# Performance work log

Hardware: AMD Instinct MI355X
Metric: run time of the kernel (lower is better)

## Reference

```python
import jax, jax.numpy as jnp
import numpy as np

IN_F = 128
OUT_F = 64
ALPHA = 0.2  # LeakyReLU negative slope


def setup_inputs() -> dict:
    key = jax.random.key(0)
    k1, k2, k3 = jax.random.split(key, 3)
    B, N = 8, 2048
    inp = jax.random.normal(k1, (B, N, IN_F), dtype=jnp.float32)
    adj = jnp.ones((B, N, N), dtype=jnp.float32)  # unused by the layer (no masking)
    # Parameters (xavier_uniform-style scale)
    w_lim = np.sqrt(6.0 / (IN_F + OUT_F))
    W = jax.random.uniform(k2, (OUT_F, IN_F), minval=-w_lim, maxval=w_lim, dtype=jnp.float32)
    a_lim = np.sqrt(6.0 / (2 * OUT_F + 1))
    a = jax.random.uniform(k3, (1, 2 * OUT_F), minval=-a_lim, maxval=a_lim, dtype=jnp.float32)
    return {"input": inp, "adj": adj, "W": W, "a": a}


def reference(input, adj, W, a):
    # h = W(input): [B, N, OUT_F]
    h = jnp.einsum("bnf,of->bno", input, W)
    # a^T [h_i || h_j] = a1^T h_i + a2^T h_j  (exact decomposition of the concat trick)
    a1 = a[0, :OUT_F]
    a2 = a[0, OUT_F:]
    s1 = jnp.einsum("bno,o->bn", h, a1)  # score contribution from node i
    s2 = jnp.einsum("bno,o->bn", h, a2)  # score contribution from node j
    e = s1[:, :, None] + s2[:, None, :]  # [B, N, N]
    e = jnp.where(e >= 0, e, ALPHA * e)  # LeakyReLU
    attention = jax.nn.softmax(e, axis=2)  # softmax over neighbors j (adj is NOT used)
    h_prime = jnp.einsum("bij,bjo->bio", attention, h)
    # concat=True -> ELU
    return jax.nn.elu(h_prime)
```

## Files before the change

kernel.cpp:

```cpp
#include <hip/hip_runtime.h>
#include <cstdio>

#define ALPHA 0.2f
constexpr int NN = 2048;
constexpr int FI = 128;
constexpr int FO = 64;
constexpr int SEG = 64;
constexpr int NSEG = NN / SEG;

__global__ __launch_bounds__(256) void k_h(const float* __restrict__ inp,
    const float* __restrict__ W, const float* __restrict__ a,
    float* __restrict__ h, float* __restrict__ s1, float* __restrict__ s2)
{
  __shared__ float4 Wq[(FI / 4) * FO];
  const int t = threadIdx.x;
  const float4* Wg = (const float4*)W;
#pragma unroll
  for (int i = 0; i < 8; ++i) {
    int f = t + i * 256;
    int o = f >> 5, cq = f & 31;
    Wq[cq * FO + o] = Wg[f];
  }
  __syncthreads();
  const int lane = t & 63;
  const int wv = t >> 6;
  const size_t rowbase = ((size_t)blockIdx.x * 4 + wv) * 8;
  const float a1v = a[lane], a2v = a[FO + lane];
#pragma unroll
  for (int g = 0; g < 2; ++g) {
    const size_t r0 = rowbase + g * 4;
    const float4* x0 = (const float4*)(inp + r0 * FI);
    const float4* x1 = x0 + (FI / 4);
    const float4* x2 = x0 + 2 * (FI / 4);
    const float4* x3 = x0 + 3 * (FI / 4);
    float acc0 = 0.f, acc1 = 0.f, acc2 = 0.f, acc3 = 0.f;
#pragma unroll
    for (int cq = 0; cq < 32; ++cq) {
      float4 w = Wq[cq * FO + lane];
      float4 xa = x0[cq];
      acc0 = fmaf(xa.x, w.x, fmaf(xa.y, w.y, fmaf(xa.z, w.z, fmaf(xa.w, w.w, acc0))));
      float4 xb = x1[cq];
      acc1 = fmaf(xb.x, w.x, fmaf(xb.y, w.y, fmaf(xb.z, w.z, fmaf(xb.w, w.w, acc1))));
      float4 xc = x2[cq];
      acc2 = fmaf(xc.x, w.x, fmaf(xc.y, w.y, fmaf(xc.z, w.z, fmaf(xc.w, w.w, acc2))));
      float4 xd = x3[cq];
      acc3 = fmaf(xd.x, w.x, fmaf(xd.y, w.y, fmaf(xd.z, w.z, fmaf(xd.w, w.w, acc3))));
    }
    h[(r0 + 0) * FO + lane] = acc0;
    h[(r0 + 1) * FO + lane] = acc1;
    h[(r0 + 2) * FO + lane] = acc2;
    h[(r0 + 3) * FO + lane] = acc3;
    float p0 = acc0 * a1v, q0 = acc0 * a2v;
    float p1 = acc1 * a1v, q1 = acc1 * a2v;
    float p2 = acc2 * a1v, q2 = acc2 * a2v;
    float p3 = acc3 * a1v, q3 = acc3 * a2v;
#pragma unroll
    for (int off = 32; off; off >>= 1) {
      p0 += __shfl_down(p0, off); q0 += __shfl_down(q0, off);
      p1 += __shfl_down(p1, off); q1 += __shfl_down(q1, off);
      p2 += __shfl_down(p2, off); q2 += __shfl_down(q2, off);
      p3 += __shfl_down(p3, off); q3 += __shfl_down(q3, off);
    }
    if (lane == 0) {
      s1[r0 + 0] = p0; s2[r0 + 0] = q0;
      s1[r0 + 1] = p1; s2[r0 + 1] = q1;
      s1[r0 + 2] = p2; s2[r0 + 2] = q2;
      s1[r0 + 3] = p3; s2[r0 + 3] = q3;
    }
  }
}

__global__ __launch_bounds__(256) void k_rankA(const float* __restrict__ s2,
    int* __restrict__ part)
{
  __shared__ float ck[64];
  const int b = blockIdx.x >> 5;
  const int c = blockIdx.x & 31;
  const int t = threadIdx.x;
  if (t < 64) ck[t] = s2[b * NN + c * 64 + t];
  float v[8];
#pragma unroll
  for (int rr = 0; rr < 8; ++rr) v[rr] = s2[b * NN + rr * 256 + t];
  __syncthreads();
  int cnt[8] = {0, 0, 0, 0, 0, 0, 0, 0};
  const int j0 = c * 64;
#pragma unroll 4
  for (int jj = 0; jj < 64; ++jj) {
    const float x = ck[jj];
    const int j = j0 + jj;
#pragma unroll
    for (int rr = 0; rr < 8; ++rr) {
      const int i = rr * 256 + t;
      cnt[rr] += (x > v[rr]) || (x == v[rr] && j < i);
    }
  }
  int* pp = part + (size_t)(b * 32 + c) * NN;
#pragma unroll
  for (int rr = 0; rr < 8; ++rr) pp[rr * 256 + t] = cnt[rr];
}

__global__ __launch_bounds__(1024) void k_batch(const float* __restrict__ s2,
    const int* __restrict__ part, const float* __restrict__ s1g,
    float* __restrict__ sortedS2, int* __restrict__ sortedIdx,
    float* __restrict__ ep, float* __restrict__ eq,
    float* __restrict__ Zp, float* __restrict__ Zq,
    int* __restrict__ kArr, float* __restrict__ m2g)
{
  __shared__ float ssv[NN];
  __shared__ int sid[NN];
  __shared__ float sep[NN], seq[NN];
  __shared__ float wt[16], wo[16];
  const int b = blockIdx.x;
  const int t = threadIdx.x;
  const int lane = t & 63;
  const int w = t >> 6;
#pragma unroll
  for (int rr = 0; rr < 2; ++rr) {
    const int i = t + rr * 1024;
    const int* pp = part + (size_t)b * 32 * NN + i;
    int rank = 0;
#pragma unroll 8
    for (int c = 0; c < 32; ++c) rank += pp[(size_t)c * NN];
    float v = s2[b * NN + i];
    ssv[rank] = v;
    sid[rank] = i;
  }
  __syncthreads();
  const float m2 = ssv[0];
  if (t == 0) m2g[b] = m2;
#pragma unroll
  for (int rr = 0; rr < 2; ++rr) {
    const int r = t + rr * 1024;
    float v = ssv[r];
    float e1 = expf(v - m2), e2 = expf(ALPHA * (v - m2));
    sep[r] = e1; seq[r] = e2;
    sortedS2[b * NN + r] = v;
    sortedIdx[b * NN + r] = sid[r];
    ep[b * NN + r] = e1;
    eq[b * NN + r] = e2;
  }
  __syncthreads();
  float a0 = sep[2 * t], a1 = sep[2 * t + 1];
  float l = a0 + a1;
  float incl = l;
#pragma unroll
  for (int off = 1; off < 64; off <<= 1) {
    float x = __shfl_up(incl, off);
    if (lane >= off) incl += x;
  }
  if (lane == 63) wt[w] = incl;
  __syncthreads();
  if (t < 16) {
    float v = wt[t];
    float wi = v;
#pragma unroll
    for (int off = 1; off < 16; off <<= 1) {
      float x = __shfl_up(wi, off);
      if (t >= off) wi += x;
    }
    wo[t] = wi - v;
  }
  __syncthreads();
  {
    float excl = wo[w] + (incl - l);
    Zp[b * (NN + 1) + 2 * t] = excl;
    Zp[b * (NN + 1) + 2 * t + 1] = excl + a0;
    if (t == 1023) Zp[b * (NN + 1) + NN] = excl + l;
  }
  __syncthreads();
  float b0 = seq[NN - 1 - 2 * t], b1 = seq[NN - 2 - 2 * t];
  float l2 = b0 + b1;
  float incl2 = l2;
#pragma unroll
  for (int off = 1; off < 64; off <<= 1) {
    float x = __shfl_up(incl2, off);
    if (lane >= off) incl2 += x;
  }
  if (lane == 63) wt[w] = incl2;
  __syncthreads();
  if (t < 16) {
    float v = wt[t];
    float wi = v;
#pragma unroll
    for (int off = 1; off < 16; off <<= 1) {
      float x = __shfl_up(wi, off);
      if (t >= off) wi += x;
    }
    wo[t] = wi - v;
  }
  __syncthreads();
  {
    float excl = wo[w] + (incl2 - l2);
    Zq[b * (NN + 1) + NN - 1 - 2 * t] = excl + b0;
    Zq[b * (NN + 1) + NN - 2 - 2 * t] = excl + l2;
    if (t == 0) Zq[b * (NN + 1) + NN] = 0.f;
  }
#pragma unroll
  for (int rr = 0; rr < 2; ++rr) {
    const int i = 2 * t + rr;
    const float thr = -s1g[b * NN + i];
    int lo = 0, hi = NN;
    while (lo < hi) {
      int mid = (lo + hi) >> 1;
      if (ssv[mid] >= thr) lo = mid + 1; else hi = mid;
    }
    kArr[b * NN + i] = lo;
  }
}

__global__ __launch_bounds__(256) void k_seg(const float* __restrict__ h,
    const int* __restrict__ sortedIdx, const float* __restrict__ ep,
    const float* __restrict__ eq,
    float* __restrict__ Lp, float* __restrict__ Lq,
    float* __restrict__ segTotP, float* __restrict__ segTotQ)
{
  const int lane = threadIdx.x & 63;
  const int s = blockIdx.x * 4 + (threadIdx.x >> 6);
  const int b = s >> 5;
  const int base = b * NN + (s & (NSEG - 1)) * SEG;
  float vq[SEG];
  float runP = 0.f;
#pragma unroll
  for (int r = 0; r < SEG; ++r) {
    int idx = sortedIdx[base + r];
    float hv = h[((size_t)(b * NN + idx)) * FO + lane];
    runP = fmaf(ep[base + r], hv, runP);
    Lp[(size_t)(base + r) * FO + lane] = runP;
    vq[r] = eq[base + r] * hv;
  }
  segTotP[(size_t)s * FO + lane] = runP;
  float runQ = 0.f;
#pragma unroll
  for (int r = SEG - 1; r >= 0; --r) {
    runQ += vq[r];
    Lq[(size_t)(base + r) * FO + lane] = runQ;
  }
  segTotQ[(size_t)s * FO + lane] = runQ;
}

__global__ __launch_bounds__(256) void k_out(const float* __restrict__ s1g,
    const int* __restrict__ kArr,
    const float* __restrict__ Lp, const float* __restrict__ Lq,
    const float* __restrict__ Zp, const float* __restrict__ Zq,
    const float* __restrict__ segTotP, const float* __restrict__ segTotQ,
    const float* __restrict__ m2g, float* __restrict__ out)
{
  __shared__ float cp[NSEG][FO];
  __shared__ float cq[NSEG][FO];
  const int t = threadIdx.x;
  const int b = blockIdx.x >> 7;
  const float* stP = segTotP + (size_t)b * NSEG * FO;
  const float* stQ = segTotQ + (size_t)b * NSEG * FO;
#pragma unroll
  for (int i = 0; i < NSEG * FO / 256; ++i) {
    ((float*)cp)[t + i * 256] = stP[t + i * 256];
    ((float*)cq)[t + i * 256] = stQ[t + i * 256];
  }
  __syncthreads();
  if (t < 64) {
    float run = 0.f;
    for (int ss = 0; ss < NSEG; ++ss) { run += cp[ss][t]; cp[ss][t] = run; }
  } else if (t < 128) {
    int o = t - 64;
    float run = 0.f;
    for (int ss = NSEG - 1; ss >= 0; --ss) { run += cq[ss][o]; cq[ss][o] = run; }
  }
  __syncthreads();
  const int lane = t & 63;
  const int wv = t >> 6;
  const float m2 = m2g[b];
#pragma unroll
  for (int rr = 0; rr < 4; ++rr) {
    const int i = (blockIdx.x & 127) * 16 + wv * 4 + rr;
    const int gi = b * NN + i;
    const int k = kArr[gi];
    const float s1v = s1g[gi];
    const float u = s1v + m2;
    const float c = fmaxf(u, ALPHA * u);
    const float wp = expf(u - c);
    const float wq = expf(ALPHA * u - c);
    const float zp = Zp[b * (NN + 1) + k];
    const float zq = Zq[b * (NN + 1) + k];
    float P = 0.f, Q = 0.f;
    if (k > 0) {
      int sP = (k - 1) >> 6;
      P = (sP > 0 ? cp[sP - 1][lane] : 0.f) +
          Lp[((size_t)b * NN + (k - 1)) * FO + lane];
    }
    if (k < NN) {
      int sQ = k >> 6;
      Q = (sQ < NSEG - 1 ? cq[sQ + 1][lane] : 0.f) +
          Lq[((size_t)b * NN + k) * FO + lane];
    }
    const float v = (wp * P + wq * Q) / (wp * zp + wq * zq);
    out[(size_t)gi * FO + lane] = (v > 0.f) ? v : expm1f(v);
  }
}

extern "C" void kernel_launch(void* const* d_in, const int* in_sizes, int n_in,
                              void* d_out, int out_size, void* d_ws, size_t ws_size,
                              hipStream_t stream) {
  const float* inp = (const float*)d_in[0];
  const float* W = (const float*)d_in[2];
  const float* a = (const float*)d_in[3];
  float* out = (float*)d_out;

  constexpr size_t NH = (size_t)8 * NN * FO;
  constexpr size_t NR = (size_t)8 * NN;
  constexpr size_t NZ = (size_t)8 * (NN + 1);
  constexpr size_t NST = (size_t)8 * NSEG * FO;
  constexpr size_t needFloats = 3 * NH + 7 * NR + 2 * NZ + 2 * NST + 8 + 32 * NR;
  if (ws_size < needFloats * sizeof(float)) {
    fprintf(stderr, "kernel_launch: ws too small (%zu < %zu)\n",
            ws_size, needFloats * sizeof(float));
    return;
  }
  float* ws = (float*)d_ws;
  float* h        = ws;
  float* Lp       = h + NH;
  float* Lq       = Lp + NH;
  float* s1       = Lq + NH;
  float* s2       = s1 + NR;
  float* sortedS2 = s2 + NR;
  int*   sortedIdx= (int*)(sortedS2 + NR);
  float* ep       = (float*)(sortedIdx + NR);
  float* eq       = ep + NR;
  int*   kArr     = (int*)(eq + NR);
  float* Zp       = (float*)(kArr + NR);
  float* Zq       = Zp + NZ;
  float* segTotP  = Zq + NZ;
  float* segTotQ  = segTotP + NST;
  float* m2       = segTotQ + NST;
  int*   part     = (int*)(m2 + 8);

  k_h<<<512, 256, 0, stream>>>(inp, W, a, h, s1, s2);
  k_rankA<<<256, 256, 0, stream>>>(s2, part);
  k_batch<<<8, 1024, 0, stream>>>(s2, part, s1, sortedS2, sortedIdx, ep, eq,
                                  Zp, Zq, kArr, m2);
  k_seg<<<64, 256, 0, stream>>>(h, sortedIdx, ep, eq, Lp, Lq, segTotP, segTotQ);
  k_out<<<1024, 256, 0, stream>>>(s1, kArr, Lp, Lq, Zp, Zq,
                                  segTotP, segTotQ, m2, out);
}
```

Before: 66.80 us.

## Shrink scan segments to raise parallelism in segmented prefix-sum kernels

Reduces the segment length of the sorted prefix-sum pass from 64 to 16, so k_seg launches four times as many waves, each with a much shorter serial chain, and front-loads all gathered loads before the scans. k_out now scans the larger segment-total table with all four waves using a two-level scan instead of two serial threads, and processes twice as many rows per block with half the blocks. The unused sortedS2 write is dropped from k_batch. The trade-off is a larger segment-total table to load and scan in every k_out block, plus more register arrays per thread in k_seg.

```diff
diff --git a/kernel.cpp b/kernel.cpp
--- a/kernel.cpp
+++ b/kernel.cpp
@@ -5,7 +5,7 @@
 constexpr int NN = 2048;
 constexpr int FI = 128;
 constexpr int FO = 64;
-constexpr int SEG = 64;
+constexpr int SEG = 16;
 constexpr int NSEG = NN / SEG;
 
 __global__ __launch_bounds__(256) void k_h(const float* __restrict__ inp,
@@ -101,7 +101,7 @@
 
 __global__ __launch_bounds__(1024) void k_batch(const float* __restrict__ s2,
     const int* __restrict__ part, const float* __restrict__ s1g,
-    float* __restrict__ sortedS2, int* __restrict__ sortedIdx,
+    int* __restrict__ sortedIdx,
     float* __restrict__ ep, float* __restrict__ eq,
     float* __restrict__ Zp, float* __restrict__ Zq,
     int* __restrict__ kArr, float* __restrict__ m2g)
@@ -134,7 +134,6 @@
     float v = ssv[r];
     float e1 = expf(v - m2), e2 = expf(ALPHA * (v - m2));
     sep[r] = e1; seq[r] = e2;
-    sortedS2[b * NN + r] = v;
     sortedIdx[b * NN + r] = sid[r];
     ep[b * NN + r] = e1;
     eq[b * NN + r] = e2;
@@ -216,26 +215,30 @@
 {
   const int lane = threadIdx.x & 63;
   const int s = blockIdx.x * 4 + (threadIdx.x >> 6);
-  const int b = s >> 5;
+  const int b = s >> 7;
   const int base = b * NN + (s & (NSEG - 1)) * SEG;
-  float vq[SEG];
-  float runP = 0.f;
+  float hv[SEG], wp[SEG], wq[SEG];
 #pragma unroll
   for (int r = 0; r < SEG; ++r) {
     int idx = sortedIdx[base + r];
-    float hv = h[((size_t)(b * NN + idx)) * FO + lane];
-    runP = fmaf(ep[base + r], hv, runP);
-    Lp[(size_t)(base + r) * FO + lane] = runP;
-    vq[r] = eq[base + r] * hv;
-  }
-  segTotP[(size_t)s * FO + lane] = runP;
-  float runQ = 0.f;
+    hv[r] = h[((size_t)(b * NN + idx)) * FO + lane];
+  }
+#pragma unroll
+  for (int r = 0; r < SEG; ++r) { wp[r] = ep[base + r]; wq[r] = eq[base + r]; }
+  float run = 0.f;
+#pragma unroll
+  for (int r = 0; r < SEG; ++r) {
+    run = fmaf(wp[r], hv[r], run);
+    Lp[(size_t)(base + r) * FO + lane] = run;
+  }
+  segTotP[(size_t)s * FO + lane] = run;
+  run = 0.f;
 #pragma unroll
   for (int r = SEG - 1; r >= 0; --r) {
-    runQ += vq[r];
-    Lq[(size_t)(base + r) * FO + lane] = runQ;
-  }
-  segTotQ[(size_t)s * FO + lane] = runQ;
+    run = fmaf(wq[r], hv[r], run);
+    Lq[(size_t)(base + r) * FO + lane] = run;
+  }
+  segTotQ[(size_t)s * FO + lane] = run;
 }
 
 __global__ __launch_bounds__(256) void k_out(const float* __restrict__ s1g,
@@ -247,31 +250,44 @@
 {
   __shared__ float cp[NSEG][FO];
   __shared__ float cq[NSEG][FO];
+  __shared__ float qtP[4][FO], qtQ[4][FO];
   const int t = threadIdx.x;
-  const int b = blockIdx.x >> 7;
-  const float* stP = segTotP + (size_t)b * NSEG * FO;
-  const float* stQ = segTotQ + (size_t)b * NSEG * FO;
-#pragma unroll
-  for (int i = 0; i < NSEG * FO / 256; ++i) {
-    ((float*)cp)[t + i * 256] = stP[t + i * 256];
-    ((float*)cq)[t + i * 256] = stQ[t + i * 256];
-  }
-  __syncthreads();
-  if (t < 64) {
+  const int b = blockIdx.x >> 6;
+  const float4* stP = (const float4*)(segTotP + (size_t)b * NSEG * FO);
+  const float4* stQ = (const float4*)(segTotQ + (size_t)b * NSEG * FO);
+  float4* cpv = (float4*)cp;
+  float4* cqv = (float4*)cq;
+#pragma unroll
+  for (int i = 0; i < NSEG * FO / 4 / 256; ++i) {
+    cpv[t + i * 256] = stP[t + i * 256];
+    cqv[t + i * 256] = stQ[t + i * 256];
+  }
+  __syncthreads();
+  const int o = t & 63;
+  const int q = t >> 6;
+  {
     float run = 0.f;
-    for (int ss = 0; ss < NSEG; ++ss) { run += cp[ss][t]; cp[ss][t] = run; }
-  } else if (t < 128) {
-    int o = t - 64;
-    float run = 0.f;
-    for (int ss = NSEG - 1; ss >= 0; --ss) { run += cq[ss][o]; cq[ss][o] = run; }
-  }
-  __syncthreads();
-  const int lane = t & 63;
-  const int wv = t >> 6;
+    for (int s = q * 32; s < q * 32 + 32; ++s) { run += cp[s][o]; cp[s][o] = run; }
+    qtP[q][o] = run;
+    run = 0.f;
+    for (int s = q * 32 + 31; s >= q * 32; --s) { run += cq[s][o]; cq[s][o] = run; }
+    qtQ[q][o] = run;
+  }
+  __syncthreads();
+  {
+    float offP = 0.f;
+    for (int q2 = 0; q2 < q; ++q2) offP += qtP[q2][o];
+    float offQ = 0.f;
+    for (int q2 = q + 1; q2 < 4; ++q2) offQ += qtQ[q2][o];
+    for (int s = q * 32; s < q * 32 + 32; ++s) { cp[s][o] += offP; cq[s][o] += offQ; }
+  }
+  __syncthreads();
+  const int lane = o;
+  const int wv = q;
   const float m2 = m2g[b];
 #pragma unroll
-  for (int rr = 0; rr < 4; ++rr) {
-    const int i = (blockIdx.x & 127) * 16 + wv * 4 + rr;
+  for (int rr = 0; rr < 8; ++rr) {
+    const int i = (blockIdx.x & 63) * 32 + wv * 8 + rr;
     const int gi = b * NN + i;
     const int k = kArr[gi];
     const float s1v = s1g[gi];
@@ -283,12 +299,12 @@
     const float zq = Zq[b * (NN + 1) + k];
     float P = 0.f, Q = 0.f;
     if (k > 0) {
-      int sP = (k - 1) >> 6;
+      int sP = (k - 1) >> 4;
       P = (sP > 0 ? cp[sP - 1][lane] : 0.f) +
           Lp[((size_t)b * NN + (k - 1)) * FO + lane];
     }
     if (k < NN) {
-      int sQ = k >> 6;
+      int sQ = k >> 4;
       Q = (sQ < NSEG - 1 ? cq[sQ + 1][lane] : 0.f) +
           Lq[((size_t)b * NN + k) * FO + lane];
     }
@@ -309,7 +325,7 @@
   constexpr size_t NR = (size_t)8 * NN;
   constexpr size_t NZ = (size_t)8 * (NN + 1);
   constexpr size_t NST = (size_t)8 * NSEG * FO;
-  constexpr size_t needFloats = 3 * NH + 7 * NR + 2 * NZ + 2 * NST + 8 + 32 * NR;
+  constexpr size_t needFloats = 3 * NH + 6 * NR + 2 * NZ + 2 * NST + 8 + 32 * NR;
   if (ws_size < needFloats * sizeof(float)) {
     fprintf(stderr, "kernel_launch: ws too small (%zu < %zu)\n",
             ws_size, needFloats * sizeof(float));
@@ -321,8 +337,7 @@
   float* Lq       = Lp + NH;
   float* s1       = Lq + NH;
   float* s2       = s1 + NR;
-  float* sortedS2 = s2 + NR;
-  int*   sortedIdx= (int*)(sortedS2 + NR);
+  int*   sortedIdx= (int*)(s2 + NR);
   float* ep       = (float*)(sortedIdx + NR);
   float* eq       = ep + NR;
   int*   kArr     = (int*)(eq + NR);
@@ -335,9 +350,9 @@
 
   k_h<<<512, 256, 0, stream>>>(inp, W, a, h, s1, s2);
   k_rankA<<<256, 256, 0, stream>>>(s2, part);
-  k_batch<<<8, 1024, 0, stream>>>(s2, part, s1, sortedS2, sortedIdx, ep, eq,
+  k_batch<<<8, 1024, 0, stream>>>(s2, part, s1, sortedIdx, ep, eq,
                                   Zp, Zq, kArr, m2);
-  k_seg<<<64, 256, 0, stream>>>(h, sortedIdx, ep, eq, Lp, Lq, segTotP, segTotQ);
-  k_out<<<1024, 256, 0, stream>>>(s1, kArr, Lp, Lq, Zp, Zq,
-                                  segTotP, segTotQ, m2, out);
-}
+  k_seg<<<256, 256, 0, stream>>>(h, sortedIdx, ep, eq, Lp, Lq, segTotP, segTotQ);
+  k_out<<<512, 256, 0, stream>>>(s1, kArr, Lp, Lq, Zp, Zq,
+                                 segTotP, segTotQ, m2, out);
+}
```

Measured after the change: 75.22 us. 1.13x slower.
